# Kernel tuning notes

Measured on AMD Instinct MI355X. Metric: run time of the kernel, lower is better.

Reference implementation:

```python
import jax, jax.numpy as jnp
import numpy as np

L = 2          # num_hidden_layers
B, S, H = 2, 2048, 1024
NH, DH = 16, 64   # heads, head dim
FF = 4096
EPS = 1e-5


def setup_inputs() -> dict:
    key = jax.random.key(0)
    ks = jax.random.split(key, 20)
    s = 0.02
    inp = {
        "hidden_states": jax.random.normal(ks[0], (B, S, H), jnp.float32),
        "attention_mask": jnp.zeros((B, 1, 1, S), jnp.float32),
        "Wq": jax.random.normal(ks[1], (L, H, H), jnp.float32) * s,
        "bq": jnp.zeros((L, H), jnp.float32),
        "Wk": jax.random.normal(ks[2], (L, H, H), jnp.float32) * s,
        "bk": jnp.zeros((L, H), jnp.float32),
        "Wv": jax.random.normal(ks[3], (L, H, H), jnp.float32) * s,
        "bv": jnp.zeros((L, H), jnp.float32),
        "Wao": jax.random.normal(ks[4], (L, H, H), jnp.float32) * s,
        "bao": jnp.zeros((L, H), jnp.float32),
        "ln1_g": jnp.ones((L, H), jnp.float32),
        "ln1_b": jnp.zeros((L, H), jnp.float32),
        "Wi": jax.random.normal(ks[5], (L, H, FF), jnp.float32) * s,
        "bi": jnp.zeros((L, FF), jnp.float32),
        "Wo": jax.random.normal(ks[6], (L, FF, H), jnp.float32) * s,
        "bo": jnp.zeros((L, H), jnp.float32),
        "ln2_g": jnp.ones((L, H), jnp.float32),
        "ln2_b": jnp.zeros((L, H), jnp.float32),
    }
    return inp


def _layernorm(x, g, b):
    m = jnp.mean(x, axis=-1, keepdims=True)
    v = jnp.var(x, axis=-1, keepdims=True)
    return (x - m) * jax.lax.rsqrt(v + EPS) * g + b


def _split_heads(x):
    # [B,S,H] -> [B,NH,S,DH]
    return x.reshape(B, S, NH, DH).transpose(0, 2, 1, 3)


def _layer(x, mask, Wq, bq, Wk, bk, Wv, bv, Wao, bao, g1, b1, Wi, bi, Wo, bo, g2, b2):
    q = _split_heads(x @ Wq + bq)
    k = _split_heads(x @ Wk + bk)
    v = _split_heads(x @ Wv + bv)
    scores = jnp.einsum('bhqd,bhkd->bhqk', q, k) / np.sqrt(DH).astype(np.float32)
    scores = scores + mask  # additive attention mask
    probs = jax.nn.softmax(scores, axis=-1)
    ctx = jnp.einsum('bhqk,bhkd->bhqd', probs, v)
    ctx = ctx.transpose(0, 2, 1, 3).reshape(B, S, H)
    x = _layernorm(ctx @ Wao + bao + x, g1, b1)
    ffn = jax.nn.gelu(x @ Wi + bi, approximate=False) @ Wo + bo
    return _layernorm(ffn + x, g2, b2)


def reference(hidden_states, attention_mask, Wq, bq, Wk, bk, Wv, bv, Wao, bao,
              ln1_g, ln1_b, Wi, bi, Wo, bo, ln2_g, ln2_b):
    x = hidden_states
    for i in range(L):
        x = _layer(x, attention_mask,
                   Wq[i], bq[i], Wk[i], bk[i], Wv[i], bv[i], Wao[i], bao[i],
                   ln1_g[i], ln1_b[i], Wi[i], bi[i], Wo[i], bo[i], ln2_g[i], ln2_b[i])
    return x
```

## Files before the change

### kernel.cpp

```cpp
#include <hip/hip_runtime.h>

typedef _Float16 half_t;
typedef _Float16 half8  __attribute__((ext_vector_type(8)));
typedef _Float16 half4v __attribute__((ext_vector_type(4)));
typedef float    f32x4  __attribute__((ext_vector_type(4)));

#define AS1 __attribute__((address_space(1)))
#define AS3 __attribute__((address_space(3)))

#define MODE_H16  0
#define MODE_F32R 1
#define MODE_GELU 2

__device__ __forceinline__ f32x4 zero4() {
    f32x4 z; z[0] = 0.f; z[1] = 0.f; z[2] = 0.f; z[3] = 0.f; return z;
}

__device__ __forceinline__ half8 lds_frag(const half_t* p) {
    union { uint4 u; half8 h; } c;
    c.u = *(const uint4*)p;
    return c.h;
}

__device__ __forceinline__ float gelu_f(float v) {
    float t = v * v;
    float u = v * (1.595769122f + 0.0713548163f * t);
    return v / (1.f + __expf(-u));
}

__device__ __forceinline__ void gl_lds16(const half_t* g, half_t* l) {
    __builtin_amdgcn_global_load_lds(
        (AS1 unsigned int*)(unsigned long long)(const void*)g,
        (AS3 unsigned int*)l,
        16, 0, 0);
}


__global__ __launch_bounds__(256) void gemm_bt(
    const half_t* __restrict__ A,
    const half_t* __restrict__ Bt,
    const float*  __restrict__ bias,
    const float*  __restrict__ res,
    void* __restrict__ out,
    int M, int N, int K, int mode)
{
    __shared__ __align__(16) half_t As[128 * 64];
    __shared__ __align__(16) half_t Bs[128 * 64];

    const int tid  = threadIdx.x;
    const int w    = tid >> 6, lane = tid & 63;
    const int m0   = blockIdx.y * 128, n0 = blockIdx.x * 128;
    const int g    = lane >> 4, ml = lane & 15, m7 = ml & 7;
    const int mo   = (w >> 1) * 64, no = (w & 1) * 64;
    const int r8   = lane >> 3;
    const int sck  = ((lane & 7) ^ (r8 & 7)) * 8;

    f32x4 acc[4][4];
#pragma unroll
    for (int i = 0; i < 4; i++)
#pragma unroll
        for (int j = 0; j < 4; j++) acc[i][j] = zero4();

    const half_t* Ag = A  + (size_t)m0 * K;
    const half_t* Bg = Bt + (size_t)n0 * K;

    for (int k0 = 0; k0 < K; k0 += 64) {
        __syncthreads();
#pragma unroll
        for (int i = 0; i < 4; i++) {
            int t = w * 4 + i;
            gl_lds16(Ag + (size_t)(t * 8 + r8) * K + k0 + sck, &As[t * 512]);
            gl_lds16(Bg + (size_t)(t * 8 + r8) * K + k0 + sck, &Bs[t * 512]);
        }
        __syncthreads();
#pragma unroll
        for (int kk = 0; kk < 2; kk++) {
            const int co = ((kk * 4 + g) ^ m7) * 8;
            half8 af[4], bf[4];
#pragma unroll
            for (int i = 0; i < 4; i++) af[i] = lds_frag(&As[(mo + i * 16 + ml) * 64 + co]);
#pragma unroll
            for (int j = 0; j < 4; j++) bf[j] = lds_frag(&Bs[(no + j * 16 + ml) * 64 + co]);
#pragma unroll
            for (int i = 0; i < 4; i++)
#pragma unroll
                for (int j = 0; j < 4; j++)
                    acc[i][j] = __builtin_amdgcn_mfma_f32_16x16x32_f16(af[i], bf[j], acc[i][j], 0, 0, 0);
        }
    }

    const int gm0 = m0 + mo, gn0 = n0 + no;
#pragma unroll
    for (int j = 0; j < 4; j++) {
        int col = gn0 + j * 16 + ml;
        float bv = bias[col];
#pragma unroll
        for (int i = 0; i < 4; i++) {
#pragma unroll
            for (int r = 0; r < 4; r++) {
                int row = gm0 + i * 16 + g * 4 + r;
                float v = acc[i][j][r] + bv;
                size_t idx = (size_t)row * N + col;
                if (mode == MODE_F32R) {
                    ((float*)out)[idx] = v + res[idx];
                } else if (mode == MODE_GELU) {
                    ((half_t*)out)[idx] = (half_t)gelu_f(v);
                } else {
                    ((half_t*)out)[idx] = (half_t)v;
                }
            }
        }
    }
}

__global__ __launch_bounds__(256) void gemm_bt64(
    const half_t* __restrict__ A,
    const half_t* __restrict__ Bt,
    const float*  __restrict__ bias,
    const float*  __restrict__ res,
    float* __restrict__ out,
    int M, int N, int K)
{
    __shared__ __align__(16) half_t As[128 * 64];
    __shared__ __align__(16) half_t Bs[64 * 64];

    const int tid  = threadIdx.x;
    const int w    = tid >> 6, lane = tid & 63;
    const int m0   = blockIdx.y * 128, n0 = blockIdx.x * 64;
    const int g    = lane >> 4, ml = lane & 15, m7 = ml & 7;
    const int mo   = w * 32;
    const int r8   = lane >> 3;
    const int sck  = ((lane & 7) ^ (r8 & 7)) * 8;

    f32x4 acc[2][4];
#pragma unroll
    for (int i = 0; i < 2; i++)
#pragma unroll
        for (int j = 0; j < 4; j++) acc[i][j] = zero4();

    const half_t* Ag = A  + (size_t)m0 * K;
    const half_t* Bg = Bt + (size_t)n0 * K;

    for (int k0 = 0; k0 < K; k0 += 64) {
        __syncthreads();
#pragma unroll
        for (int i = 0; i < 4; i++) {
            int t = w * 4 + i;
            gl_lds16(Ag + (size_t)(t * 8 + r8) * K + k0 + sck, &As[t * 512]);
        }
#pragma unroll
        for (int i = 0; i < 2; i++) {
            int t = w * 2 + i;
            gl_lds16(Bg + (size_t)(t * 8 + r8) * K + k0 + sck, &Bs[t * 512]);
        }
        __syncthreads();
#pragma unroll
        for (int kk = 0; kk < 2; kk++) {
            const int co = ((kk * 4 + g) ^ m7) * 8;
            half8 af[2], bf[4];
#pragma unroll
            for (int i = 0; i < 2; i++) af[i] = lds_frag(&As[(mo + i * 16 + ml) * 64 + co]);
#pragma unroll
            for (int j = 0; j < 4; j++) bf[j] = lds_frag(&Bs[(j * 16 + ml) * 64 + co]);
#pragma unroll
            for (int i = 0; i < 2; i++)
#pragma unroll
                for (int j = 0; j < 4; j++)
                    acc[i][j] = __builtin_amdgcn_mfma_f32_16x16x32_f16(af[i], bf[j], acc[i][j], 0, 0, 0);
        }
    }

    const int gm0 = m0 + mo;
#pragma unroll
    for (int j = 0; j < 4; j++) {
        int col = n0 + j * 16 + ml;
        float bv = bias[col];
#pragma unroll
        for (int i = 0; i < 2; i++) {
#pragma unroll
            for (int r = 0; r < 4; r++) {
                int row = gm0 + i * 16 + g * 4 + r;
                size_t idx = (size_t)row * N + col;
                out[idx] = acc[i][j][r] + bv + res[idx];
            }
        }
    }
}

__global__ __launch_bounds__(256) void gemm_qkv(
    const half_t* __restrict__ A,
    const half_t* __restrict__ Bt,
    const float*  __restrict__ bq,
    const float*  __restrict__ bk,
    const float*  __restrict__ bv,
    half_t* __restrict__ Qo, half_t* __restrict__ Ko, half_t* __restrict__ Vto,
    int M, int K)
{
    __shared__ __align__(16) half_t As[128 * 64];
    __shared__ __align__(16) half_t Bs[128 * 64];

    const int tid  = threadIdx.x;
    const int w    = tid >> 6, lane = tid & 63;
    const int m0   = blockIdx.y * 128, n0 = blockIdx.x * 128;
    const int g    = lane >> 4, ml = lane & 15, m7 = ml & 7;
    const int mo   = (w >> 1) * 64, no = (w & 1) * 64;
    const int r8   = lane >> 3;
    const int sck  = ((lane & 7) ^ (r8 & 7)) * 8;

    f32x4 acc[4][4];
#pragma unroll
    for (int i = 0; i < 4; i++)
#pragma unroll
        for (int j = 0; j < 4; j++) acc[i][j] = zero4();

    const half_t* Ag = A  + (size_t)m0 * K;
    const half_t* Bg = Bt + (size_t)n0 * K;

    for (int k0 = 0; k0 < K; k0 += 64) {
        __syncthreads();
#pragma unroll
        for (int i = 0; i < 4; i++) {
            int t = w * 4 + i;
            gl_lds16(Ag + (size_t)(t * 8 + r8) * K + k0 + sck, &As[t * 512]);
            gl_lds16(Bg + (size_t)(t * 8 + r8) * K + k0 + sck, &Bs[t * 512]);
        }
        __syncthreads();
#pragma unroll
        for (int kk = 0; kk < 2; kk++) {
            const int co = ((kk * 4 + g) ^ m7) * 8;
            half8 af[4], bf[4];
#pragma unroll
            for (int i = 0; i < 4; i++) af[i] = lds_frag(&As[(mo + i * 16 + ml) * 64 + co]);
#pragma unroll
            for (int j = 0; j < 4; j++) bf[j] = lds_frag(&Bs[(no + j * 16 + ml) * 64 + co]);
#pragma unroll
            for (int i = 0; i < 4; i++)
#pragma unroll
                for (int j = 0; j < 4; j++)
                    acc[i][j] = __builtin_amdgcn_mfma_f32_16x16x32_f16(af[i], bf[j], acc[i][j], 0, 0, 0);
        }
    }

    const int seg  = n0 >> 10;
    const int nloc = (n0 & 1023) + no;
    const float* bias = (seg == 0) ? bq : (seg == 1) ? bk : bv;
    const int gm0 = m0 + mo;

    if (seg < 2) {
        half_t* O = (seg == 0) ? Qo : Ko;
#pragma unroll
        for (int j = 0; j < 4; j++) {
            int col = nloc + j * 16 + ml;
            float bvv = bias[col];
#pragma unroll
            for (int i = 0; i < 4; i++)
#pragma unroll
                for (int r = 0; r < 4; r++)
                    O[(size_t)(gm0 + i * 16 + g * 4 + r) * 1024 + col] =
                        (half_t)(acc[i][j][r] + bvv);
        }
    } else {
#pragma unroll
        for (int j = 0; j < 4; j++) {
            int col = nloc + j * 16 + ml;
            float bvv = bias[col];
#pragma unroll
            for (int i = 0; i < 4; i++) {
                int rowb = gm0 + i * 16 + g * 4;
                int bb = rowb >> 11, sl = rowb & 2047;
                half4v v;
#pragma unroll
                for (int r = 0; r < 4; r++) v[r] = (half_t)(acc[i][j][r] + bvv);
                *(half4v*)&Vto[((size_t)bb * 1024 + col) * 2048 + sl] = v;
            }
        }
    }
}

__global__ __launch_bounds__(256, 2) void flash_attn(
    const half_t* __restrict__ Q,
    const half_t* __restrict__ Kq,
    const half_t* __restrict__ Vt,
    const float*  __restrict__ mask,
    half_t* __restrict__ ctx,
    int S, int H)
{
    __shared__ __align__(16) half_t Ks[64 * 64];
    __shared__ __align__(16) half_t Vs[64 * 64];
    __shared__ __align__(16) half_t Ps[4 * 32 * 64];

    const int qt = blockIdx.x, h = blockIdx.y, b = blockIdx.z;
    const int tid = threadIdx.x, w = tid >> 6, lane = tid & 63;
    const int g = lane >> 4, ml = lane & 15, m7 = ml & 7;

    const int q0 = qt * 128 + w * 32;
    const half_t* Qg = Q  + ((size_t)(b * S + q0)) * H + h * 64;
    const half_t* Kg = Kq + ((size_t)b * S) * H + h * 64;
    const half_t* Vg = Vt + ((size_t)b * H + h * 64) * (size_t)S;
    const float*  mk = mask + (size_t)b * S;

    half8 qf[2][2];
#pragma unroll
    for (int qi = 0; qi < 2; qi++)
#pragma unroll
        for (int kk = 0; kk < 2; kk++)
            qf[qi][kk] = *(const half8*)(Qg + (size_t)(qi * 16 + ml) * H + kk * 32 + g * 8);

    float m_[2] = {-1e30f, -1e30f}, l_[2] = {0.f, 0.f};
    f32x4 o[2][4];
#pragma unroll
    for (int qi = 0; qi < 2; qi++)
#pragma unroll
        for (int df = 0; df < 4; df++) o[qi][df] = zero4();

    half_t* Pw = &Ps[w * 32 * 64];
    const int srow = tid >> 3;
    const int sc   = tid & 7;

    for (int kv0 = 0; kv0 < S; kv0 += 64) {
        __syncthreads();
#pragma unroll
        for (int t = 0; t < 2; t++) {
            int row = t * 32 + srow;
            int ck  = sc ^ (row & 7);
            gl_lds16(Kg + (size_t)(kv0 + row) * H + ck * 8, &Ks[(t * 256 + w * 64) * 8]);
            gl_lds16(Vg + (size_t)row * S + kv0 + ck * 8,   &Vs[(t * 256 + w * 64) * 8]);
        }
        __syncthreads();

        f32x4 s[2][4];
#pragma unroll
        for (int kvf = 0; kvf < 4; kvf++) {
            half8 k0 = lds_frag(&Ks[(kvf * 16 + ml) * 64 + ((0 + g) ^ m7) * 8]);
            half8 k1 = lds_frag(&Ks[(kvf * 16 + ml) * 64 + ((4 + g) ^ m7) * 8]);
            s[0][kvf] = __builtin_amdgcn_mfma_f32_16x16x32_f16(k0, qf[0][0], zero4(), 0, 0, 0);
            s[0][kvf] = __builtin_amdgcn_mfma_f32_16x16x32_f16(k1, qf[0][1], s[0][kvf], 0, 0, 0);
            s[1][kvf] = __builtin_amdgcn_mfma_f32_16x16x32_f16(k0, qf[1][0], zero4(), 0, 0, 0);
            s[1][kvf] = __builtin_amdgcn_mfma_f32_16x16x32_f16(k1, qf[1][1], s[1][kvf], 0, 0, 0);
        }
#pragma unroll
        for (int kvf = 0; kvf < 4; kvf++) {
            float4 mv = *(const float4*)(mk + kv0 + kvf * 16 + g * 4);
#pragma unroll
            for (int qi = 0; qi < 2; qi++) {
                s[qi][kvf][0] = s[qi][kvf][0] * 0.125f + mv.x;
                s[qi][kvf][1] = s[qi][kvf][1] * 0.125f + mv.y;
                s[qi][kvf][2] = s[qi][kvf][2] * 0.125f + mv.z;
                s[qi][kvf][3] = s[qi][kvf][3] * 0.125f + mv.w;
            }
        }
        float alpha[2];
#pragma unroll
        for (int qi = 0; qi < 2; qi++) {
            float mx = -1e30f;
#pragma unroll
            for (int kvf = 0; kvf < 4; kvf++)
#pragma unroll
                for (int r = 0; r < 4; r++) mx = fmaxf(mx, s[qi][kvf][r]);
            mx = fmaxf(mx, __shfl_xor(mx, 16));
            mx = fmaxf(mx, __shfl_xor(mx, 32));
            float mnew = fmaxf(m_[qi], mx);
            alpha[qi]  = __expf(m_[qi] - mnew);
            m_[qi] = mnew;
            float ps = 0.f;
#pragma unroll
            for (int kvf = 0; kvf < 4; kvf++)
#pragma unroll
                for (int r = 0; r < 4; r++) {
                    float pv = __expf(s[qi][kvf][r] - mnew);
                    s[qi][kvf][r] = pv; ps += pv;
                }
            ps += __shfl_xor(ps, 16);
            ps += __shfl_xor(ps, 32);
            l_[qi] = l_[qi] * alpha[qi] + ps;
#pragma unroll
            for (int kvf = 0; kvf < 4; kvf++) {
                half4v pk;
#pragma unroll
                for (int r = 0; r < 4; r++) pk[r] = (half_t)s[qi][kvf][r];
                *(half4v*)(Pw + (qi * 16 + ml) * 64 +
                           (((kvf * 2 + (g >> 1)) ^ m7) * 8) + (g & 1) * 4) = pk;
            }
        }
#pragma unroll
        for (int qi = 0; qi < 2; qi++) {
#pragma unroll
            for (int r = 0; r < 4; r++) {
                float a = __shfl(alpha[qi], (lane & 48) + g * 4 + r);
#pragma unroll
                for (int df = 0; df < 4; df++) o[qi][df][r] *= a;
            }
        }
#pragma unroll
        for (int kk = 0; kk < 2; kk++) {
            half8 pa0 = lds_frag(&Pw[(ml)      * 64 + ((kk * 4 + g) ^ m7) * 8]);
            half8 pa1 = lds_frag(&Pw[(16 + ml) * 64 + ((kk * 4 + g) ^ m7) * 8]);
#pragma unroll
            for (int df = 0; df < 4; df++) {
                half8 vb = lds_frag(&Vs[(df * 16 + ml) * 64 + ((kk * 4 + g) ^ m7) * 8]);
                o[0][df] = __builtin_amdgcn_mfma_f32_16x16x32_f16(pa0, vb, o[0][df], 0, 0, 0);
                o[1][df] = __builtin_amdgcn_mfma_f32_16x16x32_f16(pa1, vb, o[1][df], 0, 0, 0);
            }
        }
    }

#pragma unroll
    for (int qi = 0; qi < 2; qi++) {
        float inv = 1.f / l_[qi];
#pragma unroll
        for (int r = 0; r < 4; r++) {
            float iv = __shfl(inv, (lane & 48) + g * 4 + r);
            int row = b * S + q0 + qi * 16 + g * 4 + r;
#pragma unroll
            for (int df = 0; df < 4; df++)
                ctx[(size_t)row * H + h * 64 + df * 16 + ml] = (half_t)(o[qi][df][r] * iv);
        }
    }
}

__global__ __launch_bounds__(256) void transpose_cast(
    const float* __restrict__ W, half_t* __restrict__ Wt, int Kd, int Nd)
{
    __shared__ float tile[32][33];
    size_t zoff = (size_t)blockIdx.z * Kd * Nd;
    const float* Wz = W + zoff;
    half_t* Wtz = Wt + zoff;
    int n0 = blockIdx.x * 32, k0 = blockIdx.y * 32;
    int tx = threadIdx.x & 31, ty = threadIdx.x >> 5;
#pragma unroll
    for (int j = 0; j < 4; j++)
        tile[ty + j * 8][tx] = Wz[(size_t)(k0 + ty + j * 8) * Nd + n0 + tx];
    __syncthreads();
#pragma unroll
    for (int j = 0; j < 4; j++)
        Wtz[(size_t)(n0 + ty + j * 8) * Kd + k0 + tx] = (half_t)tile[tx][ty + j * 8];
}

__global__ __launch_bounds__(256) void transpose_qkv(
    const float* __restrict__ Wq, const float* __restrict__ Wk,
    const float* __restrict__ Wv, half_t* __restrict__ WT)
{
    __shared__ float tile[32][33];
    int z = blockIdx.z, l = z / 3, which = z % 3;
    const float* W = ((which == 0) ? Wq : (which == 1) ? Wk : Wv) + (size_t)l * 1024 * 1024;
    half_t* D = WT + ((size_t)l * 3 + which) * 1024 * 1024;
    int n0 = blockIdx.x * 32, k0 = blockIdx.y * 32;
    int tx = threadIdx.x & 31, ty = threadIdx.x >> 5;
#pragma unroll
    for (int j = 0; j < 4; j++)
        tile[ty + j * 8][tx] = W[(size_t)(k0 + ty + j * 8) * 1024 + n0 + tx];
    __syncthreads();
#pragma unroll
    for (int j = 0; j < 4; j++)
        D[(size_t)(n0 + ty + j * 8) * 1024 + k0 + tx] = (half_t)tile[tx][ty + j * 8];
}

__global__ __launch_bounds__(256) void cast_f32_f16(
    const float* __restrict__ in, half_t* __restrict__ out)
{
    int i = blockIdx.x * 256 + threadIdx.x;
    float4 v = ((const float4*)in)[i];
    half4v o; o[0] = (half_t)v.x; o[1] = (half_t)v.y; o[2] = (half_t)v.z; o[3] = (half_t)v.w;
    *(half4v*)(out + (size_t)i * 4) = o;
}

__global__ __launch_bounds__(256) void layernorm_k(
    const float* __restrict__ in,
    const float* __restrict__ gam, const float* __restrict__ bet,
    float* __restrict__ outf, half_t* __restrict__ outh)
{
    int row = blockIdx.x, tid = threadIdx.x;
    const float4 v = ((const float4*)(in + (size_t)row * 1024))[tid];
    float s = v.x + v.y + v.z + v.w;
    float q = v.x * v.x + v.y * v.y + v.z * v.z + v.w * v.w;
    for (int off = 32; off; off >>= 1) { s += __shfl_down(s, off); q += __shfl_down(q, off); }
    __shared__ float ss[4], sq[4];
    int w = tid >> 6;
    if ((tid & 63) == 0) { ss[w] = s; sq[w] = q; }
    __syncthreads();
    float S_ = ss[0] + ss[1] + ss[2] + ss[3];
    float Q_ = sq[0] + sq[1] + sq[2] + sq[3];
    float mean = S_ * (1.f / 1024.f);
    float var  = Q_ * (1.f / 1024.f) - mean * mean;
    float rstd = rsqrtf(var + 1e-5f);
    float4 gm = ((const float4*)gam)[tid];
    float4 bt = ((const float4*)bet)[tid];
    float y0 = (v.x - mean) * rstd * gm.x + bt.x;
    float y1 = (v.y - mean) * rstd * gm.y + bt.y;
    float y2 = (v.z - mean) * rstd * gm.z + bt.z;
    float y3 = (v.w - mean) * rstd * gm.w + bt.w;
    ((float4*)(outf + (size_t)row * 1024))[tid] = make_float4(y0, y1, y2, y3);
    half4v oh; oh[0] = (half_t)y0; oh[1] = (half_t)y1; oh[2] = (half_t)y2; oh[3] = (half_t)y3;
    *(half4v*)(outh + (size_t)row * 1024 + tid * 4) = oh;
}

extern "C" void kernel_launch(void* const* d_in, const int* in_sizes, int n_in,
                              void* d_out, int out_size, void* d_ws, size_t ws_size,
                              hipStream_t stream)
{
    const int Lc = 2, Bb = 2, S = 2048, Hh = 1024, NH = 16, FF = 4096;
    const int M = Bb * S;

    const float* hs   = (const float*)d_in[0];
    const float* mask = (const float*)d_in[1];
    const float* Wq   = (const float*)d_in[2];  const float* bq  = (const float*)d_in[3];
    const float* Wk   = (const float*)d_in[4];  const float* bk  = (const float*)d_in[5];
    const float* Wv   = (const float*)d_in[6];  const float* bv  = (const float*)d_in[7];
    const float* Wao  = (const float*)d_in[8];  const float* bao = (const float*)d_in[9];
    const float* g1   = (const float*)d_in[10]; const float* b1  = (const float*)d_in[11];
    const float* Wi   = (const float*)d_in[12]; const float* bi  = (const float*)d_in[13];
    const float* Wo   = (const float*)d_in[14]; const float* bo  = (const float*)d_in[15];
    const float* g2   = (const float*)d_in[16]; const float* b2  = (const float*)d_in[17];

    char* p = (char*)d_ws;
    auto take = [&](size_t bytes) { char* r = p; p += (bytes + 255) & ~(size_t)255; return r; };

    half_t* WqkvT = (half_t*)take((size_t)Lc * 3 * Hh * Hh * 2);
    half_t* WaoT  = (half_t*)take((size_t)Lc * Hh * Hh * 2);
    half_t* WiT   = (half_t*)take((size_t)Lc * Hh * FF * 2);
    half_t* WoT   = (half_t*)take((size_t)Lc * FF * Hh * 2);
    half_t* xb    = (half_t*)take((size_t)M * Hh * 2);
    half_t* Qb    = (half_t*)take((size_t)M * Hh * 2);
    half_t* Kb2   = (half_t*)take((size_t)M * Hh * 2);
    half_t* Vtb   = (half_t*)take((size_t)M * Hh * 2);
    (void)          take((size_t)M * Hh * 2);
    half_t* h1    = Qb;
    float*  t0    = (float*)take((size_t)M * Hh * 4);
    float*  x1f   = (float*)take((size_t)M * Hh * 4);
    half_t* x1b   = (half_t*)take((size_t)M * Hh * 2);

    dim3 tb(256);

    transpose_qkv<<<dim3(32, 32, Lc * 3), tb, 0, stream>>>(Wq, Wk, Wv, WqkvT);
    transpose_cast<<<dim3(32, 32, Lc), tb, 0, stream>>>(Wao, WaoT, Hh, Hh);
    transpose_cast<<<dim3(FF / 32, 32, Lc), tb, 0, stream>>>(Wi, WiT, Hh, FF);
    transpose_cast<<<dim3(32, FF / 32, Lc), tb, 0, stream>>>(Wo, WoT, FF, Hh);
    cast_f32_f16<<<dim3(M * Hh / 1024), tb, 0, stream>>>(hs, xb);

    const float* xres = hs;
    for (int l = 0; l < Lc; l++) {
        const half_t* WqkvTl = WqkvT + (size_t)l * 3 * Hh * Hh;
        const half_t* WaoTl  = WaoT  + (size_t)l * Hh * Hh;
        const half_t* WiTl   = WiT   + (size_t)l * Hh * FF;
        const half_t* WoTl   = WoT   + (size_t)l * FF * Hh;

        gemm_qkv<<<dim3(3072 / 128, M / 128), tb, 0, stream>>>(
            xb, WqkvTl, bq + l * Hh, bk + l * Hh, bv + l * Hh, Qb, Kb2, Vtb, M, Hh);

        flash_attn<<<dim3(S / 128, NH, Bb), tb, 0, stream>>>(Qb, Kb2, Vtb, mask, xb, S, Hh);

        gemm_bt64<<<dim3(Hh / 64, M / 128), tb, 0, stream>>>(
            xb, WaoTl, bao + l * Hh, xres, t0, M, Hh, Hh);
        layernorm_k<<<dim3(M), tb, 0, stream>>>(t0, g1 + l * Hh, b1 + l * Hh, x1f, x1b);

        gemm_bt<<<dim3(FF / 128, M / 128), tb, 0, stream>>>(
            x1b, WiTl, bi + l * FF, nullptr, h1, M, FF, Hh, MODE_GELU);
        gemm_bt64<<<dim3(Hh / 64, M / 128), tb, 0, stream>>>(
            h1, WoTl, bo + l * Hh, x1f, t0, M, Hh, FF);

        float* outf = (l == Lc - 1) ? (float*)d_out : x1f;
        layernorm_k<<<dim3(M), tb, 0, stream>>>(t0, g2 + l * Hh, b2 + l * Hh, outf, xb);
        xres = x1f;
    }
}
```

Measured before the change: 749.5 us.

## Split flash attention KV range in two and merge partials

Doubles the attention grid by splitting the key/value sequence into two halves, each block writing unnormalised partial outputs plus per-row max and sum. A new merge kernel combines the two halves with log-sum-exp rescaling into the context buffer. Launch bounds are raised to allow more resident blocks. This aims to fill the GPU better than the original single-wave grid, at the cost of extra partial-result traffic, a second launch, and register pressure from the tighter occupancy target.

```diff
diff --git a/kernel.cpp b/kernel.cpp
--- a/kernel.cpp
+++ b/kernel.cpp
@@ -277,21 +277,25 @@
     }
 }
 
-__global__ __launch_bounds__(256, 2) void flash_attn(
+__global__ __launch_bounds__(256, 4) void flash_attn(
     const half_t* __restrict__ Q,
     const half_t* __restrict__ Kq,
     const half_t* __restrict__ Vt,
     const float*  __restrict__ mask,
-    half_t* __restrict__ ctx,
+    half_t* __restrict__ opart,
+    float2* __restrict__ mlpart,
     int S, int H)
 {
     __shared__ __align__(16) half_t Ks[64 * 64];
     __shared__ __align__(16) half_t Vs[64 * 64];
     __shared__ __align__(16) half_t Ps[4 * 32 * 64];
 
-    const int qt = blockIdx.x, h = blockIdx.y, b = blockIdx.z;
+    const int qt = blockIdx.x, h = blockIdx.y, z = blockIdx.z;
+    const int b = z >> 1, hf = z & 1;
     const int tid = threadIdx.x, w = tid >> 6, lane = tid & 63;
     const int g = lane >> 4, ml = lane & 15, m7 = ml & 7;
+    const int NHloc = gridDim.y;
+    const int BNHS = 2 * NHloc * S;
 
     const int q0 = qt * 128 + w * 32;
     const half_t* Qg = Q  + ((size_t)(b * S + q0)) * H + h * 64;
@@ -317,7 +321,8 @@
     const int srow = tid >> 3;
     const int sc   = tid & 7;
 
-    for (int kv0 = 0; kv0 < S; kv0 += 64) {
+    const int kvbeg = hf * (S >> 1), kvend = kvbeg + (S >> 1);
+    for (int kv0 = kvbeg; kv0 < kvend; kv0 += 64) {
         __syncthreads();
 #pragma unroll
         for (int t = 0; t < 2; t++) {
@@ -404,18 +409,44 @@
         }
     }
 
+    const size_t rowbase = (size_t)hf * BNHS + ((size_t)(b * NHloc + h)) * S + q0;
 #pragma unroll
     for (int qi = 0; qi < 2; qi++) {
-        float inv = 1.f / l_[qi];
 #pragma unroll
         for (int r = 0; r < 4; r++) {
-            float iv = __shfl(inv, (lane & 48) + g * 4 + r);
-            int row = b * S + q0 + qi * 16 + g * 4 + r;
+            size_t ro = (rowbase + qi * 16 + g * 4 + r) * 64;
 #pragma unroll
             for (int df = 0; df < 4; df++)
-                ctx[(size_t)row * H + h * 64 + df * 16 + ml] = (half_t)(o[qi][df][r] * iv);
-        }
-    }
+                opart[ro + df * 16 + ml] = (half_t)o[qi][df][r];
+        }
+    }
+    if (g == 0) {
+#pragma unroll
+        for (int qi = 0; qi < 2; qi++)
+            mlpart[rowbase + qi * 16 + ml] = make_float2(m_[qi], l_[qi]);
+    }
+}
+
+__global__ __launch_bounds__(256) void flash_merge(
+    const half_t* __restrict__ opart,
+    const float2* __restrict__ mlpart,
+    half_t* __restrict__ ctx)
+{
+    int gid = blockIdx.x * 256 + threadIdx.x;
+    int row = gid >> 4, dg = (gid & 15) * 4;
+    float2 a = mlpart[row], c = mlpart[65536 + row];
+    float m  = fmaxf(a.x, c.x);
+    float w1 = __expf(a.x - m), w2 = __expf(c.x - m);
+    float inv = 1.f / (w1 * a.y + w2 * c.y);
+    half4v o1 = *(const half4v*)&opart[(size_t)row * 64 + dg];
+    half4v o2 = *(const half4v*)&opart[(size_t)(65536 + row) * 64 + dg];
+    int b = row >> 15, hq = row & 32767;
+    int h = hq >> 11, q = hq & 2047;
+    half4v o;
+#pragma unroll
+    for (int i = 0; i < 4; i++)
+        o[i] = (half_t)((w1 * (float)o1[i] + w2 * (float)o2[i]) * inv);
+    *(half4v*)&ctx[((size_t)(b * 2048 + q)) * 1024 + h * 64 + dg] = o;
 }
 
 __global__ __launch_bounds__(256) void transpose_cast(
@@ -529,6 +560,9 @@
     float*  x1f   = (float*)take((size_t)M * Hh * 4);
     half_t* x1b   = (half_t*)take((size_t)M * Hh * 2);
 
+    half_t* opart  = (half_t*)t0;
+    float2* mlpart = (float2*)x1b;
+
     dim3 tb(256);
 
     transpose_qkv<<<dim3(32, 32, Lc * 3), tb, 0, stream>>>(Wq, Wk, Wv, WqkvT);
@@ -547,7 +581,9 @@
         gemm_qkv<<<dim3(3072 / 128, M / 128), tb, 0, stream>>>(
             xb, WqkvTl, bq + l * Hh, bk + l * Hh, bv + l * Hh, Qb, Kb2, Vtb, M, Hh);
 
-        flash_attn<<<dim3(S / 128, NH, Bb), tb, 0, stream>>>(Qb, Kb2, Vtb, mask, xb, S, Hh);
+        flash_attn<<<dim3(S / 128, NH, Bb * 2), tb, 0, stream>>>(
+            Qb, Kb2, Vtb, mask, opart, mlpart, S, Hh);
+        flash_merge<<<dim3(Bb * NH * S * 16 / 256), tb, 0, stream>>>(opart, mlpart, xb);
 
         gemm_bt64<<<dim3(Hh / 64, M / 128), tb, 0, stream>>>(
             xb, WaoTl, bao + l * Hh, xres, t0, M, Hh, Hh);
```

New measurement: 717.5 us. 4.3% less time.
